# Kernel optimization log

Hardware: AMD Instinct MI355X
Metric: run time of the kernel (lower is better)

## Reference

```python
import jax, jax.numpy as jnp
import numpy as np

N_HEADS = 16

def setup_inputs() -> dict:
    key = jax.random.key(0)
    k1, k2, k3 = jax.random.split(key, 3)
    B, T, C = 4, 2048, 1024
    x = jax.random.normal(k1, (B, T, C), dtype=jnp.float32)
    w_qkv = jax.random.normal(k2, (C, 3 * C), dtype=jnp.float32) * (1.0 / np.sqrt(C))
    w_out = jax.random.normal(k3, (C, C), dtype=jnp.float32) * (1.0 / np.sqrt(C))
    return {"x": x, "w_qkv": w_qkv, "w_out": w_out}

def reference(x, w_qkv, w_out):
    B, T, C = x.shape
    H = N_HEADS
    D = C // H
    qkv = jnp.einsum('btc,cf->btf', x, w_qkv).reshape(B, T, 3, H, D)
    q, k, v = qkv[:, :, 0], qkv[:, :, 1], qkv[:, :, 2]  # [B,T,H,D]
    q = q.transpose(0, 2, 1, 3)  # [B,H,T,D]
    k = k.transpose(0, 2, 1, 3)
    v = v.transpose(0, 2, 1, 3)
    scale = 1.0 / jnp.sqrt(jnp.asarray(D, dtype=x.dtype))
    scores = jnp.einsum('bhqd,bhkd->bhqk', q, k) * scale  # [B,H,T,T]
    causal = jnp.tril(jnp.ones((T, T), dtype=bool))
    scores = jnp.where(causal[None, None], scores, jnp.asarray(-jnp.inf, dtype=scores.dtype))
    attn = jax.nn.softmax(scores, axis=-1)
    ctx = jnp.einsum('bhqk,bhkd->bhqd', attn, v)  # [B,H,T,D]
    ctx = ctx.transpose(0, 2, 1, 3).reshape(B, T, C)
    return jnp.einsum('btc,co->bto', ctx, w_out)
```

## Files before the change

### kernel.cpp

```cpp
#include <hip/hip_runtime.h>

typedef __attribute__((ext_vector_type(8))) short bf16x8;
typedef __attribute__((ext_vector_type(4))) short bf16x4;
typedef __attribute__((ext_vector_type(4))) float f32x4;
typedef __attribute__((ext_vector_type(4))) unsigned short u16x4;

#define MFMA16(a, b, c) __builtin_amdgcn_mfma_f32_16x16x32_bf16((a), (b), (c), 0, 0, 0)
#define MFMA16K16(a, b, c) __builtin_amdgcn_mfma_f32_16x16x16bf16_1k((a), (b), (c), 0, 0, 0)

__device__ __forceinline__ unsigned short f2bf(float f) {
    union { float f; unsigned int u; } x; x.f = f;
    unsigned int r = x.u + 0x7FFFu + ((x.u >> 16) & 1u);
    return (unsigned short)(r >> 16);
}
__device__ __forceinline__ unsigned int fbits(float f) {
    union { float f; unsigned int u; } x; x.f = f;
    return x.u;
}
__device__ __forceinline__ void gload_lds16(const void* g, void* l) {
    __builtin_amdgcn_global_load_lds(
        (const __attribute__((address_space(1))) unsigned int*)g,
        (__attribute__((address_space(3))) unsigned int*)l,
        16, 0, 0);
}

__global__ void cast_x(const float* __restrict__ in, unsigned short* __restrict__ hi,
                       int n) {
    int i = (blockIdx.x * blockDim.x + threadIdx.x) * 4;
    if (i >= n) return;
    float4 v = *(const float4*)(in + i);
    float vv[4] = {v.x, v.y, v.z, v.w};
    u16x4 h;
#pragma unroll
    for (int j = 0; j < 4; ++j) h[j] = f2bf(vv[j]);
    *(u16x4*)(hi + i) = h;
}

__global__ void tcast_k(const float* __restrict__ in, unsigned short* __restrict__ out,
                        int K, int N) {
    __shared__ float tile[64][65];
    int n0 = blockIdx.x * 64, k0 = blockIdx.y * 64;
    for (int i = threadIdx.x; i < 4096; i += 256) {
        int r = i >> 6, c = i & 63;
        tile[r][c] = in[(size_t)(k0 + r) * N + n0 + c];
    }
    __syncthreads();
    for (int i = threadIdx.x; i < 4096; i += 256) {
        int r = i >> 6, c = i & 63;
        out[(size_t)(n0 + r) * K + k0 + c] = f2bf(tile[c][r]);
    }
}

__global__ __launch_bounds__(256, 2) void gemm_qkv(
    const unsigned short* __restrict__ A,
    const unsigned short* __restrict__ Bt,
    unsigned short* __restrict__ qout, unsigned short* __restrict__ kout,
    unsigned short* __restrict__ vtout) {
    const int K = 1024;
    __shared__ __align__(16) unsigned short sA[128 * 64], sB[128 * 64];
    int tid = threadIdx.x, lane = tid & 63, w = tid >> 6;
    int c = lane & 15, quad = lane >> 4;
    int sw = c & 7;
    int wm = (w >> 1) * 64, wn = (w & 1) * 64;
    int m0 = blockIdx.y * 128, n0 = blockIdx.x * 128;

    f32x4 acc[4][4];
#pragma unroll
    for (int i = 0; i < 4; i++)
#pragma unroll
        for (int j = 0; j < 4; j++) acc[i][j] = (f32x4){0.f, 0.f, 0.f, 0.f};

    for (int kk = 0; kk < K; kk += 64) {
#pragma unroll
        for (int p = 0; p < 4; ++p) {
            int ch = p * 256 + tid;
            int r = ch >> 3;
            int gs = (ch & 7) ^ (r & 7);
            gload_lds16(A + (size_t)(m0 + r) * K + kk + gs * 8, &sA[ch * 8]);
            gload_lds16(Bt + (size_t)(n0 + r) * K + kk + gs * 8, &sB[ch * 8]);
        }
        __syncthreads();
#pragma unroll
        for (int ks8 = 0; ks8 < 8; ks8 += 4) {
            bf16x8 af[4], bfr[4];
#pragma unroll
            for (int mt = 0; mt < 4; ++mt)
                af[mt] = *(const bf16x8*)&sA[(wm + mt * 16 + c) * 64 +
                                             ((ks8 + quad) ^ sw) * 8];
#pragma unroll
            for (int nt = 0; nt < 4; ++nt)
                bfr[nt] = *(const bf16x8*)&sB[(wn + nt * 16 + c) * 64 +
                                              ((ks8 + quad) ^ sw) * 8];
#pragma unroll
            for (int mt = 0; mt < 4; ++mt)
#pragma unroll
                for (int nt = 0; nt < 4; ++nt)
                    acc[mt][nt] = MFMA16(af[mt], bfr[nt], acc[mt][nt]);
        }
        __syncthreads();
    }

    const float QSCALE = 0.1803368801111601f;
#pragma unroll
    for (int mt = 0; mt < 4; ++mt) {
#pragma unroll
        for (int nt = 0; nt < 4; ++nt) {
#pragma unroll
            for (int r = 0; r < 4; ++r) {
                int row = m0 + wm + mt * 16 + quad * 4 + r;
                int col = n0 + wn + nt * 16 + c;
                float v = acc[mt][nt][r];
                int which = col >> 10;
                int h = (col >> 6) & 15;
                int d = col & 63;
                int b = row >> 11;
                int t = row & 2047;
                size_t bh_ = (size_t)(b * 16 + h);
                if (which == 0)
                    qout[(bh_ * 2048 + t) * 64 + d] = f2bf(v * QSCALE);
                else if (which == 1)
                    kout[(bh_ * 2048 + t) * 64 + d] = f2bf(v);
                else
                    vtout[(bh_ * 64 + d) * 2048 + t] = f2bf(v);
            }
        }
    }
}

__global__ __launch_bounds__(256, 2) void gemm2_bt(
    const unsigned short* __restrict__ A,
    const unsigned short* __restrict__ Bt,
    float* __restrict__ out) {
    const int K = 1024, N = 1024;
    __shared__ __align__(16) unsigned short sA[128 * 64], sB[128 * 64];
    int tid = threadIdx.x, lane = tid & 63, w = tid >> 6;
    int c = lane & 15, quad = lane >> 4;
    int sw = c & 7;
    int wm = (w >> 1) * 64, wn = (w & 1) * 64;
    int m0 = blockIdx.y * 128, n0 = blockIdx.x * 128;

    f32x4 acc[4][4];
#pragma unroll
    for (int i = 0; i < 4; i++)
#pragma unroll
        for (int j = 0; j < 4; j++) acc[i][j] = (f32x4){0.f, 0.f, 0.f, 0.f};

    for (int kk = 0; kk < K; kk += 64) {
#pragma unroll
        for (int p = 0; p < 4; ++p) {
            int ch = p * 256 + tid;
            int r = ch >> 3;
            int gs = (ch & 7) ^ (r & 7);
            gload_lds16(A + (size_t)(m0 + r) * K + kk + gs * 8, &sA[ch * 8]);
            gload_lds16(Bt + (size_t)(n0 + r) * K + kk + gs * 8, &sB[ch * 8]);
        }
        __syncthreads();
#pragma unroll
        for (int ks8 = 0; ks8 < 8; ks8 += 4) {
            bf16x8 af[4], bfr[4];
#pragma unroll
            for (int mt = 0; mt < 4; ++mt)
                af[mt] = *(const bf16x8*)&sA[(wm + mt * 16 + c) * 64 +
                                             ((ks8 + quad) ^ sw) * 8];
#pragma unroll
            for (int nt = 0; nt < 4; ++nt)
                bfr[nt] = *(const bf16x8*)&sB[(wn + nt * 16 + c) * 64 +
                                              ((ks8 + quad) ^ sw) * 8];
#pragma unroll
            for (int mt = 0; mt < 4; ++mt)
#pragma unroll
                for (int nt = 0; nt < 4; ++nt)
                    acc[mt][nt] = MFMA16(af[mt], bfr[nt], acc[mt][nt]);
        }
        __syncthreads();
    }

#pragma unroll
    for (int mt = 0; mt < 4; ++mt)
#pragma unroll
        for (int nt = 0; nt < 4; ++nt)
#pragma unroll
            for (int r = 0; r < 4; ++r) {
                int row = m0 + wm + mt * 16 + quad * 4 + r;
                int col = n0 + wn + nt * 16 + c;
                out[(size_t)row * N + col] = acc[mt][nt][r];
            }
}

#define SSTR 72
__global__ __launch_bounds__(256, 2) void attn_k(
    const unsigned short* __restrict__ q,
    const unsigned short* __restrict__ k,
    const unsigned short* __restrict__ vt,
    unsigned short* __restrict__ ctx) {
    const int T = 2048, D = 64;
    __shared__ __align__(16) unsigned short sK[64 * SSTR];
    __shared__ __align__(16) unsigned short sV[64 * SSTR];

    int tid = threadIdx.x, lane = tid & 63, w = tid >> 6;
    int c = lane & 15, quad = lane >> 4;

    int j = blockIdx.x;
    int g4 = j >> 8, q4 = (j >> 4) & 15, low = j & 15;
    int jt = (g4 & 1) ? q4 : (15 - q4);
    int bh = g4 * 16 + low;
    int b = bh >> 4, hh = bh & 15;

    const unsigned short* qh = q + (size_t)bh * T * D;
    const unsigned short* kh = k + (size_t)bh * T * D;
    const unsigned short* vh = vt + (size_t)bh * D * T;

    int dv = tid >> 3, tcv = (tid & 7) * 8;
    int q0 = jt * 128;
    int nkt = 2 * jt + 2;
    int qloc = w * 16 + c;
    int qrow[2];
    qrow[0] = q0 + qloc;
    qrow[1] = qrow[0] + 64;

    bf16x8 bq[2][2];
#pragma unroll
    for (int g = 0; g < 2; ++g) {
        bq[g][0] = *(const bf16x8*)&qh[(size_t)qrow[g] * D + quad * 8];
        bq[g][1] = *(const bf16x8*)&qh[(size_t)qrow[g] * D + 32 + quad * 8];
    }

    f32x4 o[2][4];
#pragma unroll
    for (int g = 0; g < 2; ++g)
#pragma unroll
        for (int nt = 0; nt < 4; ++nt) o[g][nt] = (f32x4){0.f, 0.f, 0.f, 0.f};
    float l_i[2] = {0.f, 0.f};

    bf16x8 kr0 = *(const bf16x8*)&kh[(size_t)lane * D + w * 8];
    bf16x8 kr1 = *(const bf16x8*)&kh[(size_t)lane * D + w * 8 + 32];
    bf16x8 vr0 = *(const bf16x8*)&vh[(size_t)dv * T + tcv];
    bf16x8 vr1 = *(const bf16x8*)&vh[(size_t)(dv + 32) * T + tcv];
    *(bf16x8*)&sK[lane * SSTR + w * 8] = kr0;
    *(bf16x8*)&sK[lane * SSTR + w * 8 + 32] = kr1;
    *(bf16x8*)&sV[dv * SSTR + tcv] = vr0;
    *(bf16x8*)&sV[(dv + 32) * SSTR + tcv] = vr1;
    __syncthreads();

    for (int kt = 0; kt < nkt; ++kt) {
        int kb = kt * 64;
        if (kt + 1 < nkt) {
            int kb2 = kb + 64;
            kr0 = *(const bf16x8*)&kh[(size_t)(kb2 + lane) * D + w * 8];
            kr1 = *(const bf16x8*)&kh[(size_t)(kb2 + lane) * D + w * 8 + 32];
            vr0 = *(const bf16x8*)&vh[(size_t)dv * T + kb2 + tcv];
            vr1 = *(const bf16x8*)&vh[(size_t)(dv + 32) * T + kb2 + tcv];
        }
        bool g0_active = (kt + 1 < nkt);

        f32x4 st[2][4];
#pragma unroll
        for (int mt = 0; mt < 4; ++mt) {
            bf16x8 ak0 = *(const bf16x8*)&sK[(mt * 16 + c) * SSTR + quad * 8];
            bf16x8 ak1 = *(const bf16x8*)&sK[(mt * 16 + c) * SSTR + 32 + quad * 8];
#pragma unroll
            for (int g = 0; g < 2; ++g) {
                f32x4 z = (f32x4){0.f, 0.f, 0.f, 0.f};
                z = MFMA16(ak0, bq[g][0], z);
                z = MFMA16(ak1, bq[g][1], z);
                st[g][mt] = z;
            }
        }

        bf16x4 pf[2][4];
#pragma unroll
        for (int g = 0; g < 2; ++g) {
            if (g == 0 && !g0_active) continue;
            bool diag = (kb == q0 + (g << 6));
            if (diag) {
#pragma unroll
                for (int mt = 0; mt < 4; ++mt)
#pragma unroll
                    for (int r = 0; r < 4; ++r)
                        if (mt * 16 + quad * 4 + r > qloc) st[g][mt][r] = -1.0e30f;
            }
            float rs = 0.f;
#pragma unroll
            for (int mt = 0; mt < 4; ++mt) {
                float p0 = __builtin_exp2f(st[g][mt][0]);
                float p1 = __builtin_exp2f(st[g][mt][1]);
                float p2 = __builtin_exp2f(st[g][mt][2]);
                float p3 = __builtin_exp2f(st[g][mt][3]);
                rs += (p0 + p1) + (p2 + p3);
                unsigned int w0 = __builtin_amdgcn_perm(
                    fbits(p1) + 0x8000u, fbits(p0) + 0x8000u, 0x07060302u);
                unsigned int w1 = __builtin_amdgcn_perm(
                    fbits(p3) + 0x8000u, fbits(p2) + 0x8000u, 0x07060302u);
                uint2 pk; pk.x = w0; pk.y = w1;
                pf[g][mt] = *(bf16x4*)&pk;
            }
            l_i[g] += rs;
        }

#pragma unroll
        for (int mt = 0; mt < 4; ++mt) {
#pragma unroll
            for (int nt = 0; nt < 4; ++nt) {
                bf16x4 av = *(const bf16x4*)&sV[(nt * 16 + c) * SSTR + mt * 16 + quad * 4];
                if (g0_active) o[0][nt] = MFMA16K16(av, pf[0][mt], o[0][nt]);
                o[1][nt] = MFMA16K16(av, pf[1][mt], o[1][nt]);
            }
        }

        if (kt + 1 < nkt) {
            __syncthreads();
            *(bf16x8*)&sK[lane * SSTR + w * 8] = kr0;
            *(bf16x8*)&sK[lane * SSTR + w * 8 + 32] = kr1;
            *(bf16x8*)&sV[dv * SSTR + tcv] = vr0;
            *(bf16x8*)&sV[(dv + 32) * SSTR + tcv] = vr1;
            __syncthreads();
        }
    }

#pragma unroll
    for (int g = 0; g < 2; ++g) {
        float l = l_i[g];
        l += __shfl_xor(l, 16);
        l += __shfl_xor(l, 32);
        float inv = 1.0f / l;
#pragma unroll
        for (int nt = 0; nt < 4; ++nt) {
            u16x4 ob;
#pragma unroll
            for (int r = 0; r < 4; ++r) ob[r] = f2bf(o[g][nt][r] * inv);
            *(u16x4*)&ctx[(size_t)(b * T + qrow[g]) * 1024 + hh * 64 + nt * 16 + quad * 4] = ob;
        }
    }
}

extern "C" void kernel_launch(void* const* d_in, const int* in_sizes, int n_in,
                              void* d_out, int out_size, void* d_ws, size_t ws_size,
                              hipStream_t stream) {
    const float* x     = (const float*)d_in[0];
    const float* w_qkv = (const float*)d_in[1];
    const float* w_out = (const float*)d_in[2];
    float* out = (float*)d_out;

    char* ws = (char*)d_ws;
    unsigned short* wqkvt = (unsigned short*)(ws + 0);
    unsigned short* woutt = (unsigned short*)(ws + 6291456);
    unsigned short* x_bf  = (unsigned short*)(ws + 8388608);
    unsigned short* qb    = (unsigned short*)(ws + 25165824);
    unsigned short* kb    = (unsigned short*)(ws + 41943040);
    unsigned short* vtb   = (unsigned short*)(ws + 58720256);
    unsigned short* ctx   = (unsigned short*)(ws + 8388608);

    cast_x<<<8192, 256, 0, stream>>>(x, x_bf, 8388608);
    tcast_k<<<dim3(48, 16), 256, 0, stream>>>(w_qkv, wqkvt, 1024, 3072);
    tcast_k<<<dim3(16, 16), 256, 0, stream>>>(w_out, woutt, 1024, 1024);
    gemm_qkv<<<dim3(24, 64), 256, 0, stream>>>(x_bf, wqkvt, qb, kb, vtb);
    attn_k<<<1024, 256, 0, stream>>>(qb, kb, vtb, ctx);
    gemm2_bt<<<dim3(8, 64), 256, 0, stream>>>(ctx, woutt, out);
}
```

Before: 298.2 us.

## Double-buffer K/V tiles in attention, drop one barrier, raise occupancy and MFMA priority

The attention kernel now keeps two LDS buffers for K and V. The next tile is written into the alternate buffer, so only one __syncthreads per iteration is needed instead of two. Launch bounds go from 2 to 4 blocks per CU, which asks the compiler to limit registers for higher occupancy. s_setprio is raised around the MFMA sections. Doubling LDS use and tighter register limits could cause spills or cap the achievable occupancy.

```diff
diff --git a/kernel.cpp b/kernel.cpp
--- a/kernel.cpp
+++ b/kernel.cpp
@@ -188,14 +188,14 @@
 }
 
 #define SSTR 72
-__global__ __launch_bounds__(256, 2) void attn_k(
+__global__ __launch_bounds__(256, 4) void attn_k(
     const unsigned short* __restrict__ q,
     const unsigned short* __restrict__ k,
     const unsigned short* __restrict__ vt,
     unsigned short* __restrict__ ctx) {
     const int T = 2048, D = 64;
-    __shared__ __align__(16) unsigned short sK[64 * SSTR];
-    __shared__ __align__(16) unsigned short sV[64 * SSTR];
+    __shared__ __align__(16) unsigned short sK[2][64 * SSTR];
+    __shared__ __align__(16) unsigned short sV[2][64 * SSTR];
 
     int tid = threadIdx.x, lane = tid & 63, w = tid >> 6;
     int c = lane & 15, quad = lane >> 4;
@@ -236,12 +236,13 @@
     bf16x8 kr1 = *(const bf16x8*)&kh[(size_t)lane * D + w * 8 + 32];
     bf16x8 vr0 = *(const bf16x8*)&vh[(size_t)dv * T + tcv];
     bf16x8 vr1 = *(const bf16x8*)&vh[(size_t)(dv + 32) * T + tcv];
-    *(bf16x8*)&sK[lane * SSTR + w * 8] = kr0;
-    *(bf16x8*)&sK[lane * SSTR + w * 8 + 32] = kr1;
-    *(bf16x8*)&sV[dv * SSTR + tcv] = vr0;
-    *(bf16x8*)&sV[(dv + 32) * SSTR + tcv] = vr1;
+    *(bf16x8*)&sK[0][lane * SSTR + w * 8] = kr0;
+    *(bf16x8*)&sK[0][lane * SSTR + w * 8 + 32] = kr1;
+    *(bf16x8*)&sV[0][dv * SSTR + tcv] = vr0;
+    *(bf16x8*)&sV[0][(dv + 32) * SSTR + tcv] = vr1;
     __syncthreads();
 
+    int cur = 0;
     for (int kt = 0; kt < nkt; ++kt) {
         int kb = kt * 64;
         if (kt + 1 < nkt) {
@@ -253,11 +254,15 @@
         }
         bool g0_active = (kt + 1 < nkt);
 
+        const unsigned short* sKc = sK[cur];
+        const unsigned short* sVc = sV[cur];
+
         f32x4 st[2][4];
+        __builtin_amdgcn_s_setprio(1);
 #pragma unroll
         for (int mt = 0; mt < 4; ++mt) {
-            bf16x8 ak0 = *(const bf16x8*)&sK[(mt * 16 + c) * SSTR + quad * 8];
-            bf16x8 ak1 = *(const bf16x8*)&sK[(mt * 16 + c) * SSTR + 32 + quad * 8];
+            bf16x8 ak0 = *(const bf16x8*)&sKc[(mt * 16 + c) * SSTR + quad * 8];
+            bf16x8 ak1 = *(const bf16x8*)&sKc[(mt * 16 + c) * SSTR + 32 + quad * 8];
 #pragma unroll
             for (int g = 0; g < 2; ++g) {
                 f32x4 z = (f32x4){0.f, 0.f, 0.f, 0.f};
@@ -266,6 +271,7 @@
                 st[g][mt] = z;
             }
         }
+        __builtin_amdgcn_s_setprio(0);
 
         bf16x4 pf[2][4];
 #pragma unroll
@@ -297,23 +303,26 @@
             l_i[g] += rs;
         }
 
+        __builtin_amdgcn_s_setprio(1);
 #pragma unroll
         for (int mt = 0; mt < 4; ++mt) {
 #pragma unroll
             for (int nt = 0; nt < 4; ++nt) {
-                bf16x4 av = *(const bf16x4*)&sV[(nt * 16 + c) * SSTR + mt * 16 + quad * 4];
+                bf16x4 av = *(const bf16x4*)&sVc[(nt * 16 + c) * SSTR + mt * 16 + quad * 4];
                 if (g0_active) o[0][nt] = MFMA16K16(av, pf[0][mt], o[0][nt]);
                 o[1][nt] = MFMA16K16(av, pf[1][mt], o[1][nt]);
             }
         }
+        __builtin_amdgcn_s_setprio(0);
 
         if (kt + 1 < nkt) {
+            int nxt = cur ^ 1;
+            *(bf16x8*)&sK[nxt][lane * SSTR + w * 8] = kr0;
+            *(bf16x8*)&sK[nxt][lane * SSTR + w * 8 + 32] = kr1;
+            *(bf16x8*)&sV[nxt][dv * SSTR + tcv] = vr0;
+            *(bf16x8*)&sV[nxt][(dv + 32) * SSTR + tcv] = vr1;
             __syncthreads();
-            *(bf16x8*)&sK[lane * SSTR + w * 8] = kr0;
-            *(bf16x8*)&sK[lane * SSTR + w * 8 + 32] = kr1;
-            *(bf16x8*)&sV[dv * SSTR + tcv] = vr0;
-            *(bf16x8*)&sV[(dv + 32) * SSTR + tcv] = vr1;
-            __syncthreads();
+            cur = nxt;
         }
     }
 
```

Result: faster. 266.7 us (-10.6%).
